# Kernel optimization log

Measured on AMD Instinct MI355X. Metric: run time of the kernel, lower is better.

## Reference

```python
import jax, jax.numpy as jnp
import numpy as np

K_FRAC = 0.5  # init arg k (keep fraction)


def setup_inputs() -> dict:
    key = jax.random.key(0)
    k1, k2, k3, k4, k5 = jax.random.split(key, 5)
    B, N, F = 1, 100000, 128
    E, Fe = 1600000, 32
    x = jax.random.normal(k1, (B, N, F), jnp.float32)
    edge_index = jax.random.randint(k2, (2, E), 0, N, dtype=jnp.int32)
    edge_attr = jax.random.normal(k3, (B, E, Fe), jnp.float32)
    # nn.Linear(in_dim, 1) params
    proj_w = jax.random.normal(k4, (1, F), jnp.float32) / jnp.sqrt(F)
    proj_b = jax.random.normal(k5, (1,), jnp.float32) * 0.01
    return {"x": x, "edge_attr": edge_attr, "proj_w": proj_w,
            "proj_b": proj_b, "edge_index": edge_index}


def reference(x, edge_attr, proj_w, proj_b, edge_index):
    B, N, F = x.shape
    # linear score + sigmoid (dropout p=0 -> identity)
    scores = jax.nn.sigmoid(jnp.einsum('bnf,of->bno', x, proj_w)[..., 0] + proj_b[0])  # [B,N]
    # torch.kthvalue(scores, kth, dim=1): kth smallest (1-indexed)
    kth = int((1.0 - K_FRAC) * N)
    kth_scores = jnp.sort(scores, axis=1)[:, kth - 1:kth]  # [B,1]
    mask = scores >= kth_scores  # [B,N]
    n_keep = int(N * K_FRAC)
    # stable descending sort of mask.float() -> true indices first, in original order
    pool_indices = jnp.argsort(jnp.where(mask, 0, 1), axis=1)[:, :n_keep]  # [B,n_keep]
    new_x = jnp.take_along_axis(x, pool_indices[..., None], axis=1)  # [B,n_keep,F]
    # 1-D node mask shared across batch (as in the torch code)
    node_mask = jnp.zeros((N,), bool).at[pool_indices].set(True)
    pool_edges = node_mask[edge_index[0]] & node_mask[edge_index[1]]  # [E] bool
    new_edge_index = edge_index[:, pool_edges]        # [2, E'] (data-dependent, eager)
    new_edge_attr = edge_attr[:, pool_edges]          # [B, E', Fe]
    mapping = jnp.full((N,), -1, jnp.int32).at[pool_indices].set(
        jnp.broadcast_to(jnp.arange(n_keep, dtype=jnp.int32), pool_indices.shape))
    new_edge_index_ordered = mapping[new_edge_index]
    return (new_x, new_edge_index, new_edge_index_ordered, new_edge_attr,
            pool_indices, pool_edges)
```

## Files before the change

### kernel.cpp

```cpp
#include <hip/hip_runtime.h>
#include <math.h>

__global__ __launch_bounds__(256) void scores_kernel(
    const float* __restrict__ x, const float* __restrict__ w,
    const float* __restrict__ bptr, int N, int F, unsigned* __restrict__ scores) {
  int node = blockIdx.x * 4 + (threadIdx.x >> 6);
  int lane = threadIdx.x & 63;
  if (node >= N) return;
  const float* xr = x + (size_t)node * F;
  double acc = 0.0;
  for (int f = lane; f < F; f += 64)
    acc += (double)xr[f] * (double)w[f];
  for (int off = 32; off > 0; off >>= 1)
    acc += __shfl_down(acc, off, 64);
  if (lane == 0) {
    double z = acc + (double)bptr[0];
    double s = 1.0 / (1.0 + exp(-z));
    scores[node] = __float_as_uint((float)s);
  }
}

__global__ __launch_bounds__(256) void hist_kernel(
    const unsigned* __restrict__ scores, int N, unsigned* __restrict__ hist,
    const unsigned* __restrict__ sel, int pass) {
  int i = blockIdx.x * 256 + threadIdx.x;
  if (i >= N) return;
  unsigned bits = scores[i];
  if (pass == 0) {
    atomicAdd(&hist[bits >> 16], 1u);
  } else {
    if ((bits >> 16) == sel[0]) atomicAdd(&hist[bits & 0xFFFFu], 1u);
  }
}

__global__ __launch_bounds__(256) void select_kernel(
    const unsigned* __restrict__ hist, const unsigned* __restrict__ qptr, unsigned qconst,
    unsigned* __restrict__ outB, unsigned* __restrict__ outRem) {
  __shared__ unsigned tot[256];
  __shared__ unsigned bins[256];
  __shared__ unsigned sChunk, sRem;
  int t = threadIdx.x;
  unsigned q = qptr ? *qptr : qconst;
  const unsigned* hp = hist + t * 256;
  unsigned s = 0;
  for (int j = 0; j < 256; j++) s += hp[j];
  tot[t] = s;
  __syncthreads();
  if (t == 0) {
    unsigned cum = 0; int c = 0;
    for (; c < 256; c++) { if (q < cum + tot[c]) break; cum += tot[c]; }
    sChunk = (unsigned)c; sRem = q - cum;
  }
  __syncthreads();
  bins[t] = hist[sChunk * 256 + t];
  __syncthreads();
  if (t == 0) {
    unsigned cum = 0; unsigned q2 = sRem; int bi = 0;
    for (; bi < 256; bi++) { if (q2 < cum + bins[bi]) break; cum += bins[bi]; }
    *outB = sChunk * 256 + bi;
    *outRem = q2 - cum;
  }
}

__global__ __launch_bounds__(256) void node_mask_sums(
    const unsigned* __restrict__ scores, const unsigned* __restrict__ sel, int N,
    unsigned* __restrict__ sums) {
  int i = blockIdx.x * 256 + threadIdx.x;
  unsigned T = (sel[0] << 16) | sel[2];
  int m = (i < N) && (scores[i] >= T);
  unsigned long long bal = __ballot(m);
  __shared__ unsigned wv[4];
  int lane = threadIdx.x & 63, wave = threadIdx.x >> 6;
  if (lane == 0) wv[wave] = (unsigned)__popcll(bal);
  __syncthreads();
  if (threadIdx.x == 0) sums[blockIdx.x] = wv[0] + wv[1] + wv[2] + wv[3];
}

__global__ __launch_bounds__(256) void scan_exclusive(unsigned* __restrict__ data, int n) {
  __shared__ unsigned tmp[256];
  __shared__ unsigned carry;
  int t = threadIdx.x;
  if (t == 0) carry = 0;
  __syncthreads();
  for (int base = 0; base < n; base += 256) {
    int i = base + t;
    unsigned v = (i < n) ? data[i] : 0;
    tmp[t] = v;
    __syncthreads();
    for (int s = 1; s < 256; s <<= 1) {
      unsigned a = (t >= s) ? tmp[t - s] : 0;
      __syncthreads();
      tmp[t] += a;
      __syncthreads();
    }
    unsigned incl = tmp[t];
    unsigned c = carry;
    if (i < n) data[i] = c + incl - v;
    unsigned total = tmp[255];
    __syncthreads();
    if (t == 0) carry = c + total;
    __syncthreads();
  }
}

__global__ __launch_bounds__(256) void node_finalize(
    const unsigned* __restrict__ scores, const unsigned* __restrict__ sel,
    const unsigned* __restrict__ sums_ex, int N, int n_keep,
    int* __restrict__ map, int* __restrict__ poolsrc, float* __restrict__ out_pool) {
  int i = blockIdx.x * 256 + threadIdx.x;
  unsigned T = (sel[0] << 16) | sel[2];
  int m = (i < N) && (scores[i] >= T);
  unsigned long long bal = __ballot(m);
  int lane = threadIdx.x & 63, wave = threadIdx.x >> 6;
  __shared__ unsigned wv[4];
  if (lane == 0) wv[wave] = (unsigned)__popcll(bal);
  __syncthreads();
  unsigned pre = 0;
  for (int k = 0; k < wave; k++) pre += wv[k];
  pre += (unsigned)__popcll(bal & ((1ull << lane) - 1ull));
  if (i < N) {
    int mv = -1;
    if (m) {
      unsigned rank = sums_ex[blockIdx.x] + pre;
      if (rank < (unsigned)n_keep) {
        mv = (int)rank;
        poolsrc[rank] = i;
        out_pool[rank] = (float)i;
      }
    }
    map[i] = mv;
  }
}

__global__ __launch_bounds__(256) void gather_x(
    const float* __restrict__ x, const int* __restrict__ poolsrc, int n_keep, int F, int N,
    float* __restrict__ outx) {
  int r = blockIdx.x * 4 + (threadIdx.x >> 6);
  int lane = threadIdx.x & 63;
  if (r >= n_keep) return;
  int src = poolsrc[r];
  src = src < 0 ? 0 : (src >= N ? N - 1 : src);
  const float2* s = (const float2*)(x + (size_t)src * F);
  float2* d = (float2*)(outx + (size_t)r * F);
  int half = F / 2;
  for (int j = lane; j < half; j += 64) d[j] = s[j];
}

__global__ __launch_bounds__(256) void edge_mask_sums(
    const int* __restrict__ ei, const int* __restrict__ map, int E,
    float* __restrict__ out_pe, unsigned* __restrict__ sums) {
  int e = blockIdx.x * 256 + threadIdx.x;
  int m = 0;
  if (e < E) {
    int a = ei[e], b = ei[E + e];
    m = (map[a] >= 0) && (map[b] >= 0);
    out_pe[e] = m ? 1.0f : 0.0f;
  }
  unsigned long long bal = __ballot(m);
  __shared__ unsigned wv[4];
  int lane = threadIdx.x & 63, wave = threadIdx.x >> 6;
  if (lane == 0) wv[wave] = (unsigned)__popcll(bal);
  __syncthreads();
  if (threadIdx.x == 0) sums[blockIdx.x] = wv[0] + wv[1] + wv[2] + wv[3];
}

__global__ __launch_bounds__(256) void edge_finalize(
    const int* __restrict__ ei, const int* __restrict__ map,
    const unsigned* __restrict__ sums_ex, int E, int Ek, int Fe,
    const float* __restrict__ attr, float* __restrict__ out,
    size_t o_ei, size_t o_eio, size_t o_attr) {
  int e = blockIdx.x * 256 + threadIdx.x;
  int m = 0, a = 0, b = 0, ma = -1, mb = -1;
  if (e < E) {
    a = ei[e]; b = ei[E + e];
    ma = map[a]; mb = map[b];
    m = (ma >= 0) && (mb >= 0);
  }
  unsigned long long bal = __ballot(m);
  int lane = threadIdx.x & 63, wave = threadIdx.x >> 6;
  __shared__ unsigned wv[4];
  if (lane == 0) wv[wave] = (unsigned)__popcll(bal);
  __syncthreads();
  unsigned pre = 0;
  for (int k = 0; k < wave; k++) pre += wv[k];
  pre += (unsigned)__popcll(bal & ((1ull << lane) - 1ull));
  if (m) {
    unsigned p = sums_ex[blockIdx.x] + pre;
    out[o_ei + p]              = (float)a;
    out[o_ei + (size_t)Ek + p] = (float)b;
    out[o_eio + p]              = (float)ma;
    out[o_eio + (size_t)Ek + p] = (float)mb;
    float4* dst = (float4*)(out + o_attr + (size_t)p * Fe);
    const float4* src = (const float4*)(attr + (size_t)e * Fe);
    for (int j = 0; j < Fe / 4; j++) dst[j] = src[j];
  }
}

extern "C" void kernel_launch(void* const* d_in, const int* in_sizes, int n_in,
                              void* d_out, int out_size, void* d_ws, size_t ws_size,
                              hipStream_t stream) {
  const int F  = in_sizes[2];
  const int E  = in_sizes[4] / 2;
  const int N  = in_sizes[0] / F;
  const int Fe = in_sizes[1] / E;
  const int n_keep = N / 2;
  const unsigned q = (unsigned)(N - n_keep - 1);
  const int Ek = (int)(((long long)out_size - (long long)n_keep * F - n_keep - E) / (4 + Fe));

  const float* x    = (const float*)d_in[0];
  const float* attr = (const float*)d_in[1];
  const float* w    = (const float*)d_in[2];
  const float* b    = (const float*)d_in[3];
  const int*   ei   = (const int*)d_in[4];
  float*       out  = (float*)d_out;

  const size_t o_newx = 0;
  const size_t o_ei   = (size_t)n_keep * F;
  const size_t o_eio  = o_ei + 2 * (size_t)Ek;
  const size_t o_attr = o_eio + 2 * (size_t)Ek;
  const size_t o_pool = o_attr + (size_t)Ek * Fe;
  const size_t o_pe   = o_pool + (size_t)n_keep;

  char* wsb = (char*)d_ws;
  size_t off = 0;
  auto carve = [&](size_t bytes) -> void* {
    void* p = wsb + off;
    off = (off + bytes + 255) & ~(size_t)255;
    return p;
  };
  const int nb_n = (N + 255) / 256;
  const int nb_e = (E + 255) / 256;
  unsigned* scores = (unsigned*)carve((size_t)N * 4);
  unsigned* hist1  = (unsigned*)carve((size_t)65536 * 4);
  unsigned* hist2  = (unsigned*)carve((size_t)65536 * 4);
  unsigned* sel    = (unsigned*)carve(64);
  unsigned* nsum   = (unsigned*)carve((size_t)nb_n * 4);
  unsigned* esum   = (unsigned*)carve((size_t)nb_e * 4);
  int* map         = (int*)carve((size_t)N * 4);
  int* poolsrc     = (int*)carve((size_t)n_keep * 4);

  hipMemsetAsync(hist1, 0, (size_t)2 * 65536 * 4, stream);
  scores_kernel<<<(N + 3) / 4, 256, 0, stream>>>(x, w, b, N, F, scores);
  hist_kernel<<<nb_n, 256, 0, stream>>>(scores, N, hist1, sel, 0);
  select_kernel<<<1, 256, 0, stream>>>(hist1, nullptr, q, sel + 0, sel + 1);
  hist_kernel<<<nb_n, 256, 0, stream>>>(scores, N, hist2, sel, 1);
  select_kernel<<<1, 256, 0, stream>>>(hist2, sel + 1, 0u, sel + 2, sel + 3);
  node_mask_sums<<<nb_n, 256, 0, stream>>>(scores, sel, N, nsum);
  scan_exclusive<<<1, 256, 0, stream>>>(nsum, nb_n);
  node_finalize<<<nb_n, 256, 0, stream>>>(scores, sel, nsum, N, n_keep, map, poolsrc, out + o_pool);
  gather_x<<<(n_keep + 3) / 4, 256, 0, stream>>>(x, poolsrc, n_keep, F, N, out + o_newx);
  edge_mask_sums<<<nb_e, 256, 0, stream>>>(ei, map, E, out + o_pe, esum);
  scan_exclusive<<<1, 256, 0, stream>>>(esum, nb_e);
  edge_finalize<<<nb_e, 256, 0, stream>>>(ei, map, esum, E, Ek, Fe, attr,
                                          out, o_ei, o_eio, o_attr);
}
```

Before: 542.4 us.

## Replace multi-pass scans with single-pass decoupled lookback compaction and fuse histogram

Node and edge compaction become single-pass kernels that use a dynamic block ticket and decoupled lookback. This replaces the separate mask-sum, single-block serial scan and finalize kernels, so edges are read once instead of twice and the slow single-block scan over about 6250 block sums is gone. The first histogram pass is folded into the score kernel, and coarse 256-bin histograms replace the 256x256 summation in select. The edge attribute copy is restaged through shared memory so that 8 threads copy each row cooperatively. The cost is spin-waiting on atomics and added contention on the histogram atomics.

New measurement: 1.577 ms. 2.91x slower.

```diff
diff --git a/kernel.cpp b/kernel.cpp
--- a/kernel.cpp
+++ b/kernel.cpp
@@ -1,9 +1,13 @@
 #include <hip/hip_runtime.h>
 #include <math.h>
 
-__global__ __launch_bounds__(256) void scores_kernel(
+#define ST_AGG 1ull
+#define ST_PRE 2ull
+
+__global__ __launch_bounds__(256) void scores_hist_kernel(
     const float* __restrict__ x, const float* __restrict__ w,
-    const float* __restrict__ bptr, int N, int F, unsigned* __restrict__ scores) {
+    const float* __restrict__ bptr, int N, int F, unsigned* __restrict__ scores,
+    unsigned* __restrict__ hist, unsigned* __restrict__ coarse) {
   int node = blockIdx.x * 4 + (threadIdx.x >> 6);
   int lane = threadIdx.x & 63;
   if (node >= N) return;
@@ -16,35 +20,35 @@
   if (lane == 0) {
     double z = acc + (double)bptr[0];
     double s = 1.0 / (1.0 + exp(-z));
-    scores[node] = __float_as_uint((float)s);
-  }
-}
-
-__global__ __launch_bounds__(256) void hist_kernel(
-    const unsigned* __restrict__ scores, int N, unsigned* __restrict__ hist,
-    const unsigned* __restrict__ sel, int pass) {
+    unsigned bits = __float_as_uint((float)s);
+    scores[node] = bits;
+    atomicAdd(&hist[bits >> 16], 1u);
+    atomicAdd(&coarse[bits >> 24], 1u);
+  }
+}
+
+__global__ __launch_bounds__(256) void hist2_kernel(
+    const unsigned* __restrict__ scores, int N, const unsigned* __restrict__ sel,
+    unsigned* __restrict__ hist, unsigned* __restrict__ coarse) {
   int i = blockIdx.x * 256 + threadIdx.x;
   if (i >= N) return;
   unsigned bits = scores[i];
-  if (pass == 0) {
-    atomicAdd(&hist[bits >> 16], 1u);
-  } else {
-    if ((bits >> 16) == sel[0]) atomicAdd(&hist[bits & 0xFFFFu], 1u);
+  if ((bits >> 16) == sel[0]) {
+    atomicAdd(&hist[bits & 0xFFFFu], 1u);
+    atomicAdd(&coarse[(bits >> 8) & 0xFFu], 1u);
   }
 }
 
 __global__ __launch_bounds__(256) void select_kernel(
-    const unsigned* __restrict__ hist, const unsigned* __restrict__ qptr, unsigned qconst,
+    const unsigned* __restrict__ coarse, const unsigned* __restrict__ fine,
+    const unsigned* __restrict__ qptr, unsigned qconst,
     unsigned* __restrict__ outB, unsigned* __restrict__ outRem) {
   __shared__ unsigned tot[256];
   __shared__ unsigned bins[256];
   __shared__ unsigned sChunk, sRem;
   int t = threadIdx.x;
   unsigned q = qptr ? *qptr : qconst;
-  const unsigned* hp = hist + t * 256;
-  unsigned s = 0;
-  for (int j = 0; j < 256; j++) s += hp[j];
-  tot[t] = s;
+  tot[t] = coarse[t];
   __syncthreads();
   if (t == 0) {
     unsigned cum = 0; int c = 0;
@@ -52,7 +56,7 @@
     sChunk = (unsigned)c; sRem = q - cum;
   }
   __syncthreads();
-  bins[t] = hist[sChunk * 256 + t];
+  bins[t] = fine[sChunk * 256 + t];
   __syncthreads();
   if (t == 0) {
     unsigned cum = 0; unsigned q2 = sRem; int bi = 0;
@@ -62,70 +66,70 @@
   }
 }
 
-__global__ __launch_bounds__(256) void node_mask_sums(
-    const unsigned* __restrict__ scores, const unsigned* __restrict__ sel, int N,
-    unsigned* __restrict__ sums) {
-  int i = blockIdx.x * 256 + threadIdx.x;
+__device__ __forceinline__ unsigned lookback_exclusive(
+    unsigned long long* status, int bid, int lane) {
+  unsigned excl = 0;
+  int j = bid - 1;
+  for (;;) {
+    int idx = j - lane;
+    unsigned long long st;
+    if (idx >= 0) {
+      do { st = atomicAdd(&status[idx], 0ull); } while ((st >> 32) == 0ull);
+    } else {
+      st = (ST_PRE << 32);
+    }
+    int isPre = ((st >> 32) == ST_PRE);
+    unsigned long long preb = __ballot(isPre);
+    int p = __ffsll(preb) - 1;
+    unsigned contrib = (p < 0 || lane <= p) ? (unsigned)st : 0u;
+    for (int off = 32; off > 0; off >>= 1)
+      contrib += __shfl_down(contrib, off, 64);
+    excl += __shfl(contrib, 0, 64);
+    if (p >= 0) return excl;
+    j -= 64;
+  }
+}
+
+__global__ __launch_bounds__(256) void node_compact(
+    const unsigned* __restrict__ scores, const unsigned* __restrict__ sel,
+    int N, int n_keep,
+    unsigned* __restrict__ ticket, unsigned long long* __restrict__ status,
+    int* __restrict__ map, int* __restrict__ poolsrc, float* __restrict__ out_pool) {
+  __shared__ unsigned sBid;
+  __shared__ unsigned wv[4];
+  __shared__ unsigned sExcl;
+  int t = threadIdx.x;
+  if (t == 0) sBid = atomicAdd(ticket, 1u);
+  __syncthreads();
+  int bid = (int)sBid;
+  int i = bid * 256 + t;
   unsigned T = (sel[0] << 16) | sel[2];
   int m = (i < N) && (scores[i] >= T);
   unsigned long long bal = __ballot(m);
-  __shared__ unsigned wv[4];
-  int lane = threadIdx.x & 63, wave = threadIdx.x >> 6;
+  int lane = t & 63, wave = t >> 6;
   if (lane == 0) wv[wave] = (unsigned)__popcll(bal);
   __syncthreads();
-  if (threadIdx.x == 0) sums[blockIdx.x] = wv[0] + wv[1] + wv[2] + wv[3];
-}
-
-__global__ __launch_bounds__(256) void scan_exclusive(unsigned* __restrict__ data, int n) {
-  __shared__ unsigned tmp[256];
-  __shared__ unsigned carry;
-  int t = threadIdx.x;
-  if (t == 0) carry = 0;
-  __syncthreads();
-  for (int base = 0; base < n; base += 256) {
-    int i = base + t;
-    unsigned v = (i < n) ? data[i] : 0;
-    tmp[t] = v;
-    __syncthreads();
-    for (int s = 1; s < 256; s <<= 1) {
-      unsigned a = (t >= s) ? tmp[t - s] : 0;
-      __syncthreads();
-      tmp[t] += a;
-      __syncthreads();
-    }
-    unsigned incl = tmp[t];
-    unsigned c = carry;
-    if (i < n) data[i] = c + incl - v;
-    unsigned total = tmp[255];
-    __syncthreads();
-    if (t == 0) carry = c + total;
-    __syncthreads();
-  }
-}
-
-__global__ __launch_bounds__(256) void node_finalize(
-    const unsigned* __restrict__ scores, const unsigned* __restrict__ sel,
-    const unsigned* __restrict__ sums_ex, int N, int n_keep,
-    int* __restrict__ map, int* __restrict__ poolsrc, float* __restrict__ out_pool) {
-  int i = blockIdx.x * 256 + threadIdx.x;
-  unsigned T = (sel[0] << 16) | sel[2];
-  int m = (i < N) && (scores[i] >= T);
-  unsigned long long bal = __ballot(m);
-  int lane = threadIdx.x & 63, wave = threadIdx.x >> 6;
-  __shared__ unsigned wv[4];
-  if (lane == 0) wv[wave] = (unsigned)__popcll(bal);
-  __syncthreads();
-  unsigned pre = 0;
+  unsigned agg = wv[0] + wv[1] + wv[2] + wv[3];
+  if (wave == 0) {
+    if (lane == 0 && bid > 0)
+      atomicExch(&status[bid], (ST_AGG << 32) | (unsigned long long)agg);
+    unsigned excl = (bid > 0) ? lookback_exclusive(status, bid, lane) : 0u;
+    if (lane == 0) {
+      atomicExch(&status[bid], (ST_PRE << 32) | (unsigned long long)(excl + agg));
+      sExcl = excl;
+    }
+  }
+  __syncthreads();
+  unsigned pre = sExcl;
   for (int k = 0; k < wave; k++) pre += wv[k];
   pre += (unsigned)__popcll(bal & ((1ull << lane) - 1ull));
   if (i < N) {
     int mv = -1;
     if (m) {
-      unsigned rank = sums_ex[blockIdx.x] + pre;
-      if (rank < (unsigned)n_keep) {
-        mv = (int)rank;
-        poolsrc[rank] = i;
-        out_pool[rank] = (float)i;
+      if (pre < (unsigned)n_keep) {
+        mv = (int)pre;
+        poolsrc[pre] = i;
+        out_pool[pre] = (float)i;
       }
     }
     map[i] = mv;
@@ -146,53 +150,63 @@
   for (int j = lane; j < half; j += 64) d[j] = s[j];
 }
 
-__global__ __launch_bounds__(256) void edge_mask_sums(
-    const int* __restrict__ ei, const int* __restrict__ map, int E,
-    float* __restrict__ out_pe, unsigned* __restrict__ sums) {
-  int e = blockIdx.x * 256 + threadIdx.x;
-  int m = 0;
-  if (e < E) {
-    int a = ei[e], b = ei[E + e];
-    m = (map[a] >= 0) && (map[b] >= 0);
-    out_pe[e] = m ? 1.0f : 0.0f;
-  }
-  unsigned long long bal = __ballot(m);
+__global__ __launch_bounds__(256) void edge_compact(
+    const int* __restrict__ ei, const int* __restrict__ map, int E, int Ek, int Fe,
+    const float* __restrict__ attr,
+    unsigned* __restrict__ ticket, unsigned long long* __restrict__ status,
+    float* __restrict__ out,
+    size_t o_ei, size_t o_eio, size_t o_attr, size_t o_pe) {
+  __shared__ unsigned sBid;
   __shared__ unsigned wv[4];
-  int lane = threadIdx.x & 63, wave = threadIdx.x >> 6;
-  if (lane == 0) wv[wave] = (unsigned)__popcll(bal);
-  __syncthreads();
-  if (threadIdx.x == 0) sums[blockIdx.x] = wv[0] + wv[1] + wv[2] + wv[3];
-}
-
-__global__ __launch_bounds__(256) void edge_finalize(
-    const int* __restrict__ ei, const int* __restrict__ map,
-    const unsigned* __restrict__ sums_ex, int E, int Ek, int Fe,
-    const float* __restrict__ attr, float* __restrict__ out,
-    size_t o_ei, size_t o_eio, size_t o_attr) {
-  int e = blockIdx.x * 256 + threadIdx.x;
+  __shared__ unsigned sExcl;
+  __shared__ int sE[256];
+  __shared__ unsigned sP[256];
+  int t = threadIdx.x;
+  if (t == 0) sBid = atomicAdd(ticket, 1u);
+  __syncthreads();
+  int bid = (int)sBid;
+  int e = bid * 256 + t;
   int m = 0, a = 0, b = 0, ma = -1, mb = -1;
   if (e < E) {
     a = ei[e]; b = ei[E + e];
     ma = map[a]; mb = map[b];
     m = (ma >= 0) && (mb >= 0);
+    out[o_pe + e] = m ? 1.0f : 0.0f;
   }
   unsigned long long bal = __ballot(m);
-  int lane = threadIdx.x & 63, wave = threadIdx.x >> 6;
-  __shared__ unsigned wv[4];
+  int lane = t & 63, wave = t >> 6;
   if (lane == 0) wv[wave] = (unsigned)__popcll(bal);
   __syncthreads();
-  unsigned pre = 0;
-  for (int k = 0; k < wave; k++) pre += wv[k];
-  pre += (unsigned)__popcll(bal & ((1ull << lane) - 1ull));
+  unsigned agg = wv[0] + wv[1] + wv[2] + wv[3];
+  if (wave == 0) {
+    if (lane == 0 && bid > 0)
+      atomicExch(&status[bid], (ST_AGG << 32) | (unsigned long long)agg);
+    unsigned excl = (bid > 0) ? lookback_exclusive(status, bid, lane) : 0u;
+    if (lane == 0) {
+      atomicExch(&status[bid], (ST_PRE << 32) | (unsigned long long)(excl + agg));
+      sExcl = excl;
+    }
+  }
+  __syncthreads();
+  unsigned wpre = 0;
+  for (int k = 0; k < wave; k++) wpre += wv[k];
+  unsigned lpre = (unsigned)__popcll(bal & ((1ull << lane) - 1ull));
+  unsigned li = wpre + lpre;
   if (m) {
-    unsigned p = sums_ex[blockIdx.x] + pre;
+    unsigned p = sExcl + li;
     out[o_ei + p]              = (float)a;
     out[o_ei + (size_t)Ek + p] = (float)b;
     out[o_eio + p]              = (float)ma;
     out[o_eio + (size_t)Ek + p] = (float)mb;
-    float4* dst = (float4*)(out + o_attr + (size_t)p * Fe);
-    const float4* src = (const float4*)(attr + (size_t)e * Fe);
-    for (int j = 0; j < Fe / 4; j++) dst[j] = src[j];
+    sE[li] = e;
+    sP[li] = p;
+  }
+  __syncthreads();
+  int fe4 = Fe >> 2;
+  for (int k = t >> 3; k < (int)agg; k += 32) {
+    const float4* src = (const float4*)(attr + (size_t)sE[k] * Fe);
+    float4* dst = (float4*)(out + o_attr + (size_t)sP[k] * Fe);
+    for (int q4 = t & 7; q4 < fe4; q4 += 8) dst[q4] = src[q4];
   }
 }
 
@@ -231,26 +245,28 @@
   const int nb_n = (N + 255) / 256;
   const int nb_e = (E + 255) / 256;
   unsigned* scores = (unsigned*)carve((size_t)N * 4);
-  unsigned* hist1  = (unsigned*)carve((size_t)65536 * 4);
-  unsigned* hist2  = (unsigned*)carve((size_t)65536 * 4);
+  size_t zero_begin = off;
+  unsigned* hist1   = (unsigned*)carve((size_t)65536 * 4);
+  unsigned* hist2   = (unsigned*)carve((size_t)65536 * 4);
+  unsigned* coarse1 = (unsigned*)carve((size_t)256 * 4);
+  unsigned* coarse2 = (unsigned*)carve((size_t)256 * 4);
+  unsigned* tickets = (unsigned*)carve(2 * 4);
+  unsigned long long* status_n = (unsigned long long*)carve((size_t)nb_n * 8);
+  unsigned long long* status_e = (unsigned long long*)carve((size_t)nb_e * 8);
+  size_t zero_end = off;
   unsigned* sel    = (unsigned*)carve(64);
-  unsigned* nsum   = (unsigned*)carve((size_t)nb_n * 4);
-  unsigned* esum   = (unsigned*)carve((size_t)nb_e * 4);
   int* map         = (int*)carve((size_t)N * 4);
   int* poolsrc     = (int*)carve((size_t)n_keep * 4);
-
-  hipMemsetAsync(hist1, 0, (size_t)2 * 65536 * 4, stream);
-  scores_kernel<<<(N + 3) / 4, 256, 0, stream>>>(x, w, b, N, F, scores);
-  hist_kernel<<<nb_n, 256, 0, stream>>>(scores, N, hist1, sel, 0);
-  select_kernel<<<1, 256, 0, stream>>>(hist1, nullptr, q, sel + 0, sel + 1);
-  hist_kernel<<<nb_n, 256, 0, stream>>>(scores, N, hist2, sel, 1);
-  select_kernel<<<1, 256, 0, stream>>>(hist2, sel + 1, 0u, sel + 2, sel + 3);
-  node_mask_sums<<<nb_n, 256, 0, stream>>>(scores, sel, N, nsum);
-  scan_exclusive<<<1, 256, 0, stream>>>(nsum, nb_n);
-  node_finalize<<<nb_n, 256, 0, stream>>>(scores, sel, nsum, N, n_keep, map, poolsrc, out + o_pool);
+  (void)ws_size;
+
+  hipMemsetAsync(hist1, 0, zero_end - zero_begin, stream);
+  scores_hist_kernel<<<(N + 3) / 4, 256, 0, stream>>>(x, w, b, N, F, scores, hist1, coarse1);
+  select_kernel<<<1, 256, 0, stream>>>(coarse1, hist1, nullptr, q, sel + 0, sel + 1);
+  hist2_kernel<<<nb_n, 256, 0, stream>>>(scores, N, sel, hist2, coarse2);
+  select_kernel<<<1, 256, 0, stream>>>(coarse2, hist2, sel + 1, 0u, sel + 2, sel + 3);
+  node_compact<<<nb_n, 256, 0, stream>>>(scores, sel, N, n_keep, tickets + 0, status_n,
+                                         map, poolsrc, out + o_pool);
   gather_x<<<(n_keep + 3) / 4, 256, 0, stream>>>(x, poolsrc, n_keep, F, N, out + o_newx);
-  edge_mask_sums<<<nb_e, 256, 0, stream>>>(ei, map, E, out + o_pe, esum);
-  scan_exclusive<<<1, 256, 0, stream>>>(esum, nb_e);
-  edge_finalize<<<nb_e, 256, 0, stream>>>(ei, map, esum, E, Ek, Fe, attr,
-                                          out, o_ei, o_eio, o_attr);
-}
+  edge_compact<<<nb_e, 256, 0, stream>>>(ei, map, E, Ek, Fe, attr, tickets + 1, status_e,
+                                         out, o_ei, o_eio, o_attr, o_pe);
+}
```
